# Optimization experiments

Hardware: AMD Instinct MI355X
Metric: run time of the kernel (lower is better)

The kernel has to match this reference:

```python
import jax, jax.numpy as jnp
import numpy as np
from functools import partial

TWO_PI = 2.0 * np.pi
H = 0.5          # frequency-grid spacing h
CG_ITERS = 50    # fixed CG iteration count (jit-friendly; matches max_cg_iter)
N_TRAIN = 100000
N_TEST = 20000
M_GRID = 64


def setup_inputs() -> dict:
    key = jax.random.key(0)
    k1, k2, k3, k4 = jax.random.split(key, 4)
    x = jax.random.uniform(k1, (N_TRAIN, 2), dtype=jnp.float32)          # nonuniform pts in [0,1]^2
    y = jax.random.normal(k2, (N_TRAIN,), dtype=jnp.float32)
    x_new = jax.random.uniform(k3, (N_TEST, 2), dtype=jnp.float32)
    # positive quadrature weights (Fourier-feature weights)
    ws = 0.5 + 0.5 * jax.random.uniform(k4, (M_GRID * M_GRID,), dtype=jnp.float32)
    sigma2 = 0.1 * jnp.ones((1,), dtype=jnp.float32)                     # noise variance
    return {"x": x, "y": y, "x_new": x_new, "ws": ws, "sigma2": sigma2, "mtot": M_GRID}


def _phase(pts_1d, freqs):
    # exp(2*pi*i * x * xi) : (N, K) complex64
    return jnp.exp(1j * (TWO_PI * pts_1d[:, None] * freqs[None, :]).astype(jnp.float32))


def _cg(A, b, iters):
    """Complex Hermitian-PD CG with fixed iteration count via lax.scan."""
    x0 = jnp.zeros_like(b)
    r0 = b
    rz0 = jnp.vdot(r0, r0).real

    def step(carry, _):
        xk, r, p, rz = carry
        Ap = A(p)
        denom = jnp.vdot(p, Ap).real
        alpha = rz / (denom + 1e-30)
        xk = xk + alpha * p
        r = r - alpha * Ap
        rz_new = jnp.vdot(r, r).real
        beta = rz_new / (rz + 1e-30)
        p = r + beta * p
        return (xk, r, p, rz_new), None

    (xk, _, _, _), _ = jax.lax.scan(step, (x0, r0, r0, rz0), None, length=iters)
    return xk


def reference(x, y, x_new, ws, sigma2, mtot):
    M = mtot
    S = 2 * M - 1
    # tensor-product frequency grid: xi_k = (k - M//2) * h per dimension
    xis_1d = (jnp.arange(M, dtype=jnp.float32) - M // 2) * H

    # ---- type-2 NUFFT adjoint (F^H y) computed separably: grid is tensor product
    E1 = _phase(x[:, 0], xis_1d)            # (N, M)
    E2 = _phase(x[:, 1], xis_1d)            # (N, M)
    Fy = jnp.einsum('na,nb->ab', jnp.conj(E1) * y[:, None].astype(jnp.complex64), jnp.conj(E2))  # (M, M)

    ws_g = ws.reshape(M, M).astype(jnp.complex64)
    rhs = ws_g * Fy                          # rhs = D F^H y

    # ---- type-1 NUFFT convolution vector v[p] = sum_n exp(2*pi*i*h*<p, x_n>), p in [-(M-1), M-1]^2
    p_1d = (jnp.arange(S, dtype=jnp.float32) - (M - 1)) * H
    G1 = _phase(x[:, 0], p_1d)              # (N, 2M-1)
    G2 = _phase(x[:, 1], p_1d)              # (N, 2M-1)
    v = jnp.einsum('na,nb->ab', G1, G2)     # (2M-1, 2M-1)
    # circularize so that index q = p mod S; v starts at p=-(M-1)
    v_circ = jnp.roll(v, shift=(-(M - 1), -(M - 1)), axis=(0, 1))
    Vf = jnp.fft.fftn(v_circ)

    def toeplitz_mv(u):                      # (T u)[k] = sum_j v[k-j] u[j], u: (M, M)
        Uf = jnp.fft.fftn(u, s=(S, S))
        full = jnp.fft.ifftn(Uf * Vf)
        return full[:M, :M]

    s2 = sigma2[0].astype(jnp.complex64)

    def A_mean(beta_flat):                   # A = D T D + sigma^2 I, acting on flat (M*M,)
        beta = beta_flat.reshape(M, M)
        out = ws_g * toeplitz_mv(ws_g * beta) + s2 * beta
        return out.reshape(-1)

    beta = _cg(A_mean, rhs.reshape(-1), CG_ITERS).reshape(M, M)

    # ---- posterior mean at test points: mu_b = Re( sum_{jk} exp(2 pi i <x_new_b, xi_jk>) * (ws*beta)[jk] )
    alpha_g = ws_g * beta                    # (M, M)
    T1 = _phase(x_new[:, 0], xis_1d)         # (B, M)
    T2 = _phase(x_new[:, 1], xis_1d)         # (B, M)
    tmp = jnp.einsum('jk,bk->bj', alpha_g, T2)   # (B, M)
    mu = jnp.real(jnp.sum(T1 * tmp, axis=1)).astype(jnp.float32)  # (B,)
    return mu
```

## Files before the change

kernel.cpp:

```cpp
#include <hip/hip_runtime.h>
#include <math.h>


typedef float f2 __attribute__((ext_vector_type(2)));
#define PB 16
#define RS 137

__device__ inline f2 f2s(float s) { return (f2){s, s}; }
__device__ inline f2 cmulf(f2 a, f2 b) {
    return (f2){a.x * b.x - a.y * b.y, a.x * b.y + a.y * b.x};
}
__device__ inline f2 cmulcf(f2 a, f2 b) {
    return (f2){a.x * b.x + a.y * b.y, a.y * b.x - a.x * b.y};
}
__device__ inline int cpad(int c) { return (c >> 4) * 17 + (c & 15); }

__device__ inline f2 phasef(float xv, float m, float scale) {
    double ang = (double)xv * (double)m;
    double r = ang - 2.0 * rint(ang * 0.5);
    float sn, cs;
    sincospif((float)r, &sn, &cs);
    return (f2){cs * scale, sn * scale};
}

__global__ __launch_bounds__(256, 2) void k_outer(const float* __restrict__ x,
                                                  const float* __restrict__ y,
                                                  float* __restrict__ pv,
                                                  float* __restrict__ pf,
                                                  int N, int cv, int cf)
{
    __shared__ f2 hs[PB][256];
    __shared__ float xs0[PB], xs1[PB], ys[PB];

    int bx = blockIdx.x;
    int t  = threadIdx.x;
    int ty = t >> 4, tx = t & 15;

    if (bx < cv) {
        int CP = (N + cv - 1) / cv;
        int n0 = bx * CP, n1 = min(N, n0 + CP);

        f2 acc[4][8];
        #pragma unroll
        for (int i = 0; i < 4; ++i)
            #pragma unroll
            for (int j = 0; j < 8; ++j) acc[i][j] = (f2){0.f, 0.f};

        for (int s = n0; s < n1; s += PB) {
            int cnt = min(PB, n1 - s);
            __syncthreads();
            if (t < cnt) {
                xs0[t] = x[2 * (s + t)];
                xs1[t] = x[2 * (s + t) + 1];
            }
            __syncthreads();
            for (int p = 0; p < cnt; ++p) {
                if (t < 192) {
                    f2 g;
                    if (t < 64)
                        g = phasef(xs0[p], (float)t, 1.f);
                    else
                        g = (t == 191) ? (f2){0.f, 0.f}
                                       : phasef(xs1[p], (float)(t - 127), 1.f);
                    hs[p][t] = g;
                }
            }
            __syncthreads();
            for (int p = 0; p < cnt; ++p) {
                f2 h1[4], h2[8], h2s[8];
                #pragma unroll
                for (int i = 0; i < 4; ++i) h1[i] = hs[p][ty * 4 + i];
                #pragma unroll
                for (int j = 0; j < 8; ++j) {
                    f2 b = hs[p][64 + tx + 16 * j];
                    h2[j] = b;
                    h2s[j] = (f2){-b.y, b.x};
                }
                #pragma unroll
                for (int i = 0; i < 4; ++i)
                    #pragma unroll
                    for (int j = 0; j < 8; ++j) {
                        acc[i][j] = acc[i][j] + f2s(h1[i].x) * h2[j];
                        acc[i][j] = acc[i][j] + f2s(h1[i].y) * h2s[j];
                    }
            }
        }
        __syncthreads();
        f2* out = (f2*)pv + (size_t)bx * 8192;
        #pragma unroll
        for (int i = 0; i < 4; ++i) {
            int a = ty * 4 + i;
            #pragma unroll
            for (int j = 0; j < 8; ++j)
                out[a * 128 + tx + 16 * j] = acc[i][j];
        }
    } else {
        int chunk = bx - cv;
        int CP = (N + cf - 1) / cf;
        int n0 = chunk * CP, n1 = min(N, n0 + CP);

        f2 acc[4][4];
        #pragma unroll
        for (int i = 0; i < 4; ++i)
            #pragma unroll
            for (int j = 0; j < 4; ++j) acc[i][j] = (f2){0.f, 0.f};

        for (int s = n0; s < n1; s += PB) {
            int cnt = min(PB, n1 - s);
            __syncthreads();
            if (t < cnt) {
                xs0[t] = x[2 * (s + t)];
                xs1[t] = x[2 * (s + t) + 1];
                ys[t]  = y[s + t];
            }
            __syncthreads();
            for (int p2 = 0; p2 < cnt; p2 += 2) {
                int p = p2 + (t >> 7);
                int c = t & 127;
                if (p < cnt) {
                    f2 g;
                    if (c < 64) g = phasef(xs0[p], (float)(32 - c), ys[p]);
                    else        g = phasef(xs1[p], (float)(32 - (c - 64)), 1.f);
                    hs[p][c] = g;
                }
            }
            __syncthreads();
            for (int p = 0; p < cnt; ++p) {
                f2 h1[4], h2[4], h2s[4];
                #pragma unroll
                for (int i = 0; i < 4; ++i) h1[i] = hs[p][ty * 4 + i];
                #pragma unroll
                for (int j = 0; j < 4; ++j) {
                    f2 b = hs[p][64 + tx + 16 * j];
                    h2[j] = b;
                    h2s[j] = (f2){-b.y, b.x};
                }
                #pragma unroll
                for (int i = 0; i < 4; ++i)
                    #pragma unroll
                    for (int j = 0; j < 4; ++j) {
                        acc[i][j] = acc[i][j] + f2s(h1[i].x) * h2[j];
                        acc[i][j] = acc[i][j] + f2s(h1[i].y) * h2s[j];
                    }
            }
        }
        __syncthreads();
        f2* out = (f2*)pf + (size_t)chunk * 4096;
        #pragma unroll
        for (int i = 0; i < 4; ++i) {
            int a = ty * 4 + i;
            #pragma unroll
            for (int j = 0; j < 4; ++j)
                out[a * 64 + tx + 16 * j] = acc[i][j];
        }
    }
}

__global__ __launch_bounds__(256) void k_reduce(const float* __restrict__ pv,
                                                const float* __restrict__ pf,
                                                const float* __restrict__ wsv,
                                                float* __restrict__ vcf,
                                                double2* __restrict__ rvec,
                                                int cv, int cf)
{
    int id = blockIdx.x * 256 + threadIdx.x;
    if (id < 65536) {
        int e = id >> 3, sl = id & 7;
        int cn = cv >> 3;
        const float* src = pv + (size_t)e * 2 + (size_t)(sl * cn) * 16384;
        float sx = 0.f, sy = 0.f;
        for (int c = 0; c < cn; ++c) { sx += src[0]; sy += src[1]; src += 16384; }
        int p1 = e >> 7, b = e & 127;
        int q2 = (b + 65) & 127;
        atomicAdd(&vcf[(p1 * 128 + q2) * 2],     sx);
        atomicAdd(&vcf[(p1 * 128 + q2) * 2 + 1], sy);
        if (p1 > 0) {
            int q1m = 128 - p1, q2m = (63 - b) & 127;
            atomicAdd(&vcf[(q1m * 128 + q2m) * 2],     sx);
            atomicAdd(&vcf[(q1m * 128 + q2m) * 2 + 1], -sy);
        }
    } else {
        int e = id - 65536;
        const float* s2p = pf + (size_t)e * 2;
        double fx = 0.0, fy2 = 0.0;
        for (int c = 0; c < cf; ++c) { fx += (double)s2p[0]; fy2 += (double)s2p[1]; s2p += 8192; }
        double w = (double)wsv[e];
        rvec[e] = make_double2(w * fx, w * fy2);
    }
}

#define TC1 0.92387953251128676f
#define TS1 0.38268343236508977f
#define TSQ 0.70710678118654752f

__device__ inline void bflyA_fwd(f2* L, const f2* tw, int b) {
    #pragma unroll
    for (int s = 0; s < 4; ++s) {
        f2 u0 = L[s], v0 = L[s + 4];
        L[s] = u0 + v0;
        L[s + 4] = cmulf(u0 - v0, tw[b + 16 * s]);
    }
    const int ss[4] = {0, 1, 4, 5};
    #pragma unroll
    for (int q = 0; q < 4; ++q) {
        int s = ss[q];
        f2 u0 = L[s], v0 = L[s + 2];
        L[s] = u0 + v0;
        L[s + 2] = cmulf(u0 - v0, tw[2 * b + 32 * (s & 1)]);
    }
    #pragma unroll
    for (int s = 0; s < 8; s += 2) {
        f2 u0 = L[s], v0 = L[s + 1];
        L[s] = u0 + v0;
        L[s + 1] = cmulf(u0 - v0, tw[4 * b]);
    }
}
__device__ inline void bflyA_inv(f2* L, const f2* tw, int b) {
    #pragma unroll
    for (int s = 0; s < 8; s += 2) {
        f2 u0 = L[s];
        f2 vw = cmulcf(L[s + 1], tw[4 * b]);
        L[s] = u0 + vw; L[s + 1] = u0 - vw;
    }
    const int ss[4] = {0, 1, 4, 5};
    #pragma unroll
    for (int q = 0; q < 4; ++q) {
        int s = ss[q];
        f2 u0 = L[s];
        f2 vw = cmulcf(L[s + 2], tw[2 * b + 32 * (s & 1)]);
        L[s] = u0 + vw; L[s + 2] = u0 - vw;
    }
    #pragma unroll
    for (int s = 0; s < 4; ++s) {
        f2 u0 = L[s];
        f2 vw = cmulcf(L[s + 4], tw[b + 16 * s]);
        L[s] = u0 + vw; L[s + 4] = u0 - vw;
    }
}
__device__ inline void bfly16_fwd(f2* M) {
    const float c8x[8]  = {1.f, TC1, TSQ, TS1, 0.f, -TS1, -TSQ, -TC1};
    const float c8y[8]  = {0.f, -TS1, -TSQ, -TC1, -1.f, -TC1, -TSQ, -TS1};
    const float c16x[4] = {1.f, TSQ, 0.f, -TSQ};
    const float c16y[4] = {0.f, -TSQ, -1.f, -TSQ};
    #pragma unroll
    for (int s = 0; s < 8; ++s) {
        f2 u0 = M[s], v0 = M[s + 8];
        M[s] = u0 + v0;
        M[s + 8] = cmulf(u0 - v0, (f2){c8x[s], c8y[s]});
    }
    #pragma unroll
    for (int q = 0; q < 8; ++q) {
        int s = (q & 3) + 8 * (q >> 2);
        f2 u0 = M[s], v0 = M[s + 4];
        M[s] = u0 + v0;
        M[s + 4] = cmulf(u0 - v0, (f2){c16x[s & 3], c16y[s & 3]});
    }
    #pragma unroll
    for (int q = 0; q < 8; ++q) {
        int s = (q & 1) + 4 * (q >> 1);
        f2 u0 = M[s], v0 = M[s + 2];
        M[s] = u0 + v0;
        f2 d = u0 - v0;
        M[s + 2] = (s & 1) ? (f2){d.y, -d.x} : d;
    }
    #pragma unroll
    for (int s = 0; s < 16; s += 2) {
        f2 u0 = M[s], v0 = M[s + 1];
        M[s] = u0 + v0; M[s + 1] = u0 - v0;
    }
}
__device__ inline void bfly16_inv(f2* M) {
    const float c8x[8]  = {1.f, TC1, TSQ, TS1, 0.f, -TS1, -TSQ, -TC1};
    const float c8y[8]  = {0.f, -TS1, -TSQ, -TC1, -1.f, -TC1, -TSQ, -TS1};
    const float c16x[4] = {1.f, TSQ, 0.f, -TSQ};
    const float c16y[4] = {0.f, -TSQ, -1.f, -TSQ};
    #pragma unroll
    for (int s = 0; s < 16; s += 2) {
        f2 u0 = M[s], v0 = M[s + 1];
        M[s] = u0 + v0; M[s + 1] = u0 - v0;
    }
    #pragma unroll
    for (int q = 0; q < 8; ++q) {
        int s = (q & 1) + 4 * (q >> 1);
        f2 u0 = M[s];
        f2 v0 = M[s + 2];
        f2 vw = (s & 1) ? (f2){-v0.y, v0.x} : v0;
        M[s] = u0 + vw; M[s + 2] = u0 - vw;
    }
    #pragma unroll
    for (int q = 0; q < 8; ++q) {
        int s = (q & 3) + 8 * (q >> 2);
        f2 u0 = M[s];
        f2 vw = cmulcf(M[s + 4], (f2){c16x[s & 3], c16y[s & 3]});
        M[s] = u0 + vw; M[s + 4] = u0 - vw;
    }
    #pragma unroll
    for (int s = 0; s < 8; ++s) {
        f2 u0 = M[s];
        f2 vw = cmulcf(M[s + 8], (f2){c8x[s], c8y[s]});
        M[s] = u0 + vw; M[s + 8] = u0 - vw;
    }
}

__device__ inline void f_rowA(f2* Z, const f2* tw, int tid, int nrows, bool zup) {
    for (int u = tid; u < nrows * 16; u += 1024) {
        int r = u >> 4, b = u & 15;
        f2* row = Z + r * RS;
        f2 L[8];
        #pragma unroll
        for (int s = 0; s < 4; ++s) L[s] = row[17 * s + b];
        if (zup) {
            #pragma unroll
            for (int s = 4; s < 8; ++s) L[s] = (f2){0.f, 0.f};
        } else {
            #pragma unroll
            for (int s = 4; s < 8; ++s) L[s] = row[17 * s + b];
        }
        bflyA_fwd(L, tw, b);
        #pragma unroll
        for (int s = 0; s < 8; ++s) row[17 * s + b] = L[s];
    }
}
__device__ inline void f_rowB(f2* Z, int tid, int nrows) {
    for (int u = tid; u < nrows * 8; u += 1024) {
        int r = u >> 3, g = u & 7;
        f2* blk = Z + r * RS + g * 17;
        f2 M[16];
        #pragma unroll
        for (int s = 0; s < 16; ++s) M[s] = blk[s];
        bfly16_fwd(M);
        #pragma unroll
        for (int s = 0; s < 16; ++s) blk[s] = M[s];
    }
}
__device__ inline void i_rowB(f2* Z, int tid, int nrows) {
    for (int u = tid; u < nrows * 8; u += 1024) {
        int r = u >> 3, g = u & 7;
        f2* blk = Z + r * RS + g * 17;
        f2 M[16];
        #pragma unroll
        for (int s = 0; s < 16; ++s) M[s] = blk[s];
        bfly16_inv(M);
        #pragma unroll
        for (int s = 0; s < 16; ++s) blk[s] = M[s];
    }
}
__device__ inline void f_colA(f2* Z, const f2* tw, int tid, bool zup) {
    for (int u = tid; u < 2048; u += 1024) {
        int c = u >> 4, b = u & 15;
        int cp = cpad(c);
        f2 L[8];
        #pragma unroll
        for (int s = 0; s < 4; ++s) L[s] = Z[(b + 16 * s) * RS + cp];
        if (zup) {
            #pragma unroll
            for (int s = 4; s < 8; ++s) L[s] = (f2){0.f, 0.f};
        } else {
            #pragma unroll
            for (int s = 4; s < 8; ++s) L[s] = Z[(b + 16 * s) * RS + cp];
        }
        bflyA_fwd(L, tw, b);
        #pragma unroll
        for (int s = 0; s < 8; ++s) Z[(b + 16 * s) * RS + cp] = L[s];
    }
}
__device__ inline void i_colA(f2* Z, const f2* tw, int tid) {
    for (int u = tid; u < 2048; u += 1024) {
        int c = u >> 4, b = u & 15;
        int cp = cpad(c);
        f2 L[8];
        #pragma unroll
        for (int s = 0; s < 8; ++s) L[s] = Z[(b + 16 * s) * RS + cp];
        bflyA_inv(L, tw, b);
        #pragma unroll
        for (int s = 0; s < 4; ++s) Z[(b + 16 * s) * RS + cp] = L[s];
    }
}
__device__ inline void f_colB(f2* Z, int tid) {
    int c = tid & 127, g = tid >> 7;
    f2* col = Z + g * 16 * RS + cpad(c);
    f2 M[16];
    #pragma unroll
    for (int s = 0; s < 16; ++s) M[s] = col[s * RS];
    bfly16_fwd(M);
    #pragma unroll
    for (int s = 0; s < 16; ++s) col[s * RS] = M[s];
}
__device__ inline void it_colB(f2* Z, const float* Vfg, int tid) {
    int c = tid & 127, g = tid >> 7;
    f2* col = Z + g * 16 * RS + cpad(c);
    const float* vf = Vfg + g * 16 * 128 + c;
    f2 M[16];
    #pragma unroll
    for (int s = 0; s < 16; ++s) M[s] = col[s * RS];
    bfly16_fwd(M);
    #pragma unroll
    for (int s = 0; s < 16; ++s) M[s] = M[s] * f2s(vf[s * 128]);
    bfly16_inv(M);
    #pragma unroll
    for (int s = 0; s < 16; ++s) col[s * RS] = M[s];
}

__device__ inline double blk_reduce(double v, double* red, int wid, int m) {
    #pragma unroll
    for (int off = 32; off > 0; off >>= 1) v += __shfl_down(v, off);
    if (m == 0) red[wid] = v;
    __syncthreads();
    double s = 0.0;
    #pragma unroll
    for (int i = 0; i < 16; ++i) s += red[i];
    return s;
}

__global__ __launch_bounds__(1024, 4) void k_cg_solve(
        const float* __restrict__ vcf, float* __restrict__ Vf,
        const double2* __restrict__ rvec, const float* __restrict__ wsv,
        const float* __restrict__ sig2, float* __restrict__ alg)
{
    __shared__ f2 Z[128 * RS];
    __shared__ f2 tw[64];
    __shared__ double redA[16], redB[16], redC[16];

    int tid = threadIdx.x;
    int wid = tid >> 6, m = tid & 63;
    int rr_ = tid >> 4, bb_ = tid & 15;

    if (tid < 64) {
        float sn, cs;
        sincospif(-(float)tid / 64.f, &sn, &cs);
        tw[tid] = (f2){cs, sn};
    }
    __syncthreads();

    for (int i = tid; i < 16384; i += 1024)
        Z[(i >> 7) * RS + cpad(i & 127)] = ((const f2*)vcf)[i];
    __syncthreads();
    f_rowA(Z, tw, tid, 128, false); __syncthreads();
    f_rowB(Z, tid, 128);            __syncthreads();
    f_colA(Z, tw, tid, false);      __syncthreads();
    f_colB(Z, tid);                 __syncthreads();
    for (int i = tid; i < 16384; i += 1024)
        Vf[i] = Z[(i >> 7) * RS + cpad(i & 127)].x * (1.f / 16384.f);
    __syncthreads();

    double2 pR[4], rR[4], xR[4];
    float wsr[4];
    double rzp = 0.0;
    #pragma unroll
    for (int s = 0; s < 4; ++s) {
        int e = rr_ * 64 + bb_ + (s << 4);
        double2 bv = rvec[e];
        pR[s] = bv; rR[s] = bv;
        xR[s] = make_double2(0.0, 0.0);
        wsr[s] = wsv[e];
        rzp += bv.x * bv.x + bv.y * bv.y;
    }
    double rz = blk_reduce(rzp, redC, wid, m);
    double s2 = (double)sig2[0];
    __syncthreads();

    for (int it = 0; it < 50; ++it) {
        {
            f2* row = Z + rr_ * RS;
            f2 L[8];
            #pragma unroll
            for (int s = 0; s < 4; ++s)
                L[s] = (f2){(float)((double)wsr[s] * pR[s].x),
                            (float)((double)wsr[s] * pR[s].y)};
            #pragma unroll
            for (int s = 4; s < 8; ++s) L[s] = (f2){0.f, 0.f};
            bflyA_fwd(L, tw, bb_);
            #pragma unroll
            for (int s = 0; s < 8; ++s) row[17 * s + bb_] = L[s];
        }
        __syncthreads();

        f_rowB(Z, tid, 64);                      __syncthreads();
        f_colA(Z, tw, tid, true);                __syncthreads();
        it_colB(Z, Vf, tid);                     __syncthreads();
        i_colA(Z, tw, tid);                      __syncthreads();
        i_rowB(Z, tid, 64);                      __syncthreads();

        f2 az[4];
        {
            f2* row = Z + rr_ * RS;
            f2 L[8];
            #pragma unroll
            for (int s = 0; s < 8; ++s) L[s] = row[17 * s + bb_];
            bflyA_inv(L, tw, bb_);
            #pragma unroll
            for (int s = 0; s < 4; ++s) az[s] = L[s];
        }
        double papp = 0.0;
        #pragma unroll
        for (int s = 0; s < 4; ++s) {
            double apx = (double)wsr[s] * (double)az[s].x + s2 * pR[s].x;
            double apy = (double)wsr[s] * (double)az[s].y + s2 * pR[s].y;
            papp += pR[s].x * apx + pR[s].y * apy;
        }
        double pap = blk_reduce(papp, redA, wid, m);
        double alpha = rz / (pap + 1e-30);

        double rrp = 0.0;
        #pragma unroll
        for (int s = 0; s < 4; ++s) {
            double apx = (double)wsr[s] * (double)az[s].x + s2 * pR[s].x;
            double apy = (double)wsr[s] * (double)az[s].y + s2 * pR[s].y;
            xR[s].x += alpha * pR[s].x; xR[s].y += alpha * pR[s].y;
            rR[s].x -= alpha * apx; rR[s].y -= alpha * apy;
            rrp += rR[s].x * rR[s].x + rR[s].y * rR[s].y;
        }
        double rzn = blk_reduce(rrp, redB, wid, m);
        double beta = rzn / (rz + 1e-30);
        rz = rzn;
        #pragma unroll
        for (int s = 0; s < 4; ++s) {
            pR[s].x = rR[s].x + beta * pR[s].x;
            pR[s].y = rR[s].y + beta * pR[s].y;
        }
    }

    #pragma unroll
    for (int s = 0; s < 4; ++s) {
        int e = rr_ * 64 + bb_ + (s << 4);
        ((f2*)alg)[e] = (f2){(float)((double)wsr[s] * xR[s].x),
                             (float)((double)wsr[s] * xR[s].y)};
    }
}

__global__ __launch_bounds__(64) void k_eval(const float* __restrict__ xnew,
                                             const float* __restrict__ alg,
                                             float* __restrict__ out, int B)
{
    __shared__ float2 al[4096];
    int t = threadIdx.x;
    int b = blockIdx.x * 64 + t;
    for (int i = t; i < 4096; i += 64) {
        f2 v = ((const f2*)alg)[i];
        al[i] = make_float2(v.x, v.y);
    }
    float x0 = 0.f, x1 = 0.f;
    if (b < B) { x0 = xnew[2 * b]; x1 = xnew[2 * b + 1]; }
    __syncthreads();
    double2 wstep; { double sn, cs; sincospi((double)x1, &sn, &cs); wstep = make_double2(cs, sn); }
    double2 e2_0;  { double sn, cs; sincospi(-32.0 * (double)x1, &sn, &cs); e2_0 = make_double2(cs, sn); }
    double2 w1;    { double sn, cs; sincospi((double)x0, &sn, &cs); w1 = make_double2(cs, sn); }
    double2 e1;    { double sn, cs; sincospi(-32.0 * (double)x0, &sn, &cs); e1 = make_double2(cs, sn); }
    double mu = 0.0;
    for (int jg = 0; jg < 4; ++jg) {
        float2 tacc[16];
        for (int q = 0; q < 16; ++q) tacc[q] = make_float2(0.f, 0.f);
        double2 e2 = e2_0;
        for (int k = 0; k < 64; ++k) {
            float2 e2f = make_float2((float)e2.x, (float)e2.y);
            for (int q = 0; q < 16; ++q) {
                int j = jg * 16 + q;
                float2 a = al[j * 64 + k];
                tacc[q].x += a.x * e2f.x - a.y * e2f.y;
                tacc[q].y += a.x * e2f.y + a.y * e2f.x;
            }
            e2 = make_double2(e2.x * wstep.x - e2.y * wstep.y,
                              e2.x * wstep.y + e2.y * wstep.x);
        }
        for (int q = 0; q < 16; ++q) {
            mu += e1.x * (double)tacc[q].x - e1.y * (double)tacc[q].y;
            e1 = make_double2(e1.x * w1.x - e1.y * w1.y,
                              e1.x * w1.y + e1.y * w1.x);
        }
    }
    if (b < B) out[b] = (float)mu;
}


extern "C" void kernel_launch(void* const* d_in, const int* in_sizes, int n_in,
                              void* d_out, int out_size, void* d_ws, size_t ws_size,
                              hipStream_t stream)
{
    const float* x    = (const float*)d_in[0];
    const float* y    = (const float*)d_in[1];
    const float* xnew = (const float*)d_in[2];
    const float* wsv  = (const float*)d_in[3];
    const float* sig2 = (const float*)d_in[4];
    int N = in_sizes[1];
    int B = in_sizes[2] / 2;

    char* base = (char*)d_ws;
    size_t o = 0;
    float*   vcf  = (float*)(base + o);   o += 131072;
    float*   Vf   = (float*)(base + o);   o += 65536;
    double2* rvec = (double2*)(base + o); o += 65536;
    float*   alg  = (float*)(base + o);   o += 32768;
    size_t avail = (ws_size > o) ? ws_size - o : 0;
    int cv = (int)(avail / 73728);
    if (cv > 768) cv = 768;
    if (cv < 16) cv = 16;
    cv &= ~15;
    int cf = cv / 4;
    float* pv = (float*)(base + o); o += (size_t)cv * 65536;
    float* pf = (float*)(base + o);

    hipMemsetAsync(vcf, 0, 131072, stream);

    k_outer<<<cv + cf, 256, 0, stream>>>(x, y, pv, pf, N, cv, cf);
    k_reduce<<<320, 256, 0, stream>>>(pv, pf, wsv, vcf, rvec, cv, cf);
    k_cg_solve<<<1, 1024, 0, stream>>>(vcf, Vf, rvec, wsv, sig2, alg);
    k_eval<<<(B + 63) / 64, 64, 0, stream>>>(xnew, alg, (float*)d_out, B);
}
```

Baseline: 1.143 ms.

## Run CG vector updates in fp32 and permute phase-table layout for contiguous reads

The CG solver's per-thread state (p, r, x) and its dot-product partials move from double to float, and the warp shuffle reductions run in float before a final double sum across waves. This is meant to cut fp64 ALU work and register pressure in the 50-iteration loop. Separately, the second-dimension phase table in the gridding kernel is stored in a permuted order so each thread reads its 8 entries contiguously. The fp32 CG may lose accuracy relative to the reference.

```diff
diff --git a/kernel.cpp b/kernel.cpp
--- a/kernel.cpp
+++ b/kernel.cpp
@@ -56,13 +56,14 @@
             __syncthreads();
             for (int p = 0; p < cnt; ++p) {
                 if (t < 192) {
-                    f2 g;
-                    if (t < 64)
-                        g = phasef(xs0[p], (float)t, 1.f);
-                    else
-                        g = (t == 191) ? (f2){0.f, 0.f}
-                                       : phasef(xs1[p], (float)(t - 127), 1.f);
-                    hs[p][t] = g;
+                    if (t < 64) {
+                        hs[p][t] = phasef(xs0[p], (float)t, 1.f);
+                    } else {
+                        int cc = t - 64;
+                        f2 g = (cc == 127) ? (f2){0.f, 0.f}
+                                           : phasef(xs1[p], (float)(cc - 63), 1.f);
+                        hs[p][64 + 8 * (cc & 15) + (cc >> 4)] = g;
+                    }
                 }
             }
             __syncthreads();
@@ -72,7 +73,7 @@
                 for (int i = 0; i < 4; ++i) h1[i] = hs[p][ty * 4 + i];
                 #pragma unroll
                 for (int j = 0; j < 8; ++j) {
-                    f2 b = hs[p][64 + tx + 16 * j];
+                    f2 b = hs[p][64 + 8 * tx + j];
                     h2[j] = b;
                     h2s[j] = (f2){-b.y, b.x};
                 }
@@ -411,6 +412,16 @@
     for (int i = 0; i < 16; ++i) s += red[i];
     return s;
 }
+__device__ inline double blk_reduce_f(float v, double* red, int wid, int m) {
+    #pragma unroll
+    for (int off = 32; off > 0; off >>= 1) v += __shfl_down(v, off);
+    if (m == 0) red[wid] = (double)v;
+    __syncthreads();
+    double s = 0.0;
+    #pragma unroll
+    for (int i = 0; i < 16; ++i) s += red[i];
+    return s;
+}
 
 __global__ __launch_bounds__(1024, 4) void k_cg_solve(
         const float* __restrict__ vcf, float* __restrict__ Vf,
@@ -443,20 +454,21 @@
         Vf[i] = Z[(i >> 7) * RS + cpad(i & 127)].x * (1.f / 16384.f);
     __syncthreads();
 
-    double2 pR[4], rR[4], xR[4];
+    f2 pR[4], rR[4], xR[4];
     float wsr[4];
-    double rzp = 0.0;
+    float rzp = 0.f;
     #pragma unroll
     for (int s = 0; s < 4; ++s) {
         int e = rr_ * 64 + bb_ + (s << 4);
         double2 bv = rvec[e];
-        pR[s] = bv; rR[s] = bv;
-        xR[s] = make_double2(0.0, 0.0);
+        f2 bf = (f2){(float)bv.x, (float)bv.y};
+        pR[s] = bf; rR[s] = bf;
+        xR[s] = (f2){0.f, 0.f};
         wsr[s] = wsv[e];
-        rzp += bv.x * bv.x + bv.y * bv.y;
-    }
-    double rz = blk_reduce(rzp, redC, wid, m);
-    double s2 = (double)sig2[0];
+        rzp += bf.x * bf.x + bf.y * bf.y;
+    }
+    double rz = blk_reduce_f(rzp, redC, wid, m);
+    float s2f = sig2[0];
     __syncthreads();
 
     for (int it = 0; it < 50; ++it) {
@@ -464,9 +476,7 @@
             f2* row = Z + rr_ * RS;
             f2 L[8];
             #pragma unroll
-            for (int s = 0; s < 4; ++s)
-                L[s] = (f2){(float)((double)wsr[s] * pR[s].x),
-                            (float)((double)wsr[s] * pR[s].y)};
+            for (int s = 0; s < 4; ++s) L[s] = f2s(wsr[s]) * pR[s];
             #pragma unroll
             for (int s = 4; s < 8; ++s) L[s] = (f2){0.f, 0.f};
             bflyA_fwd(L, tw, bb_);
@@ -481,7 +491,8 @@
         i_colA(Z, tw, tid);                      __syncthreads();
         i_rowB(Z, tid, 64);                      __syncthreads();
 
-        f2 az[4];
+        f2 ap[4];
+        float papp = 0.f;
         {
             f2* row = Z + rr_ * RS;
             f2 L[8];
@@ -489,42 +500,34 @@
             for (int s = 0; s < 8; ++s) L[s] = row[17 * s + bb_];
             bflyA_inv(L, tw, bb_);
             #pragma unroll
-            for (int s = 0; s < 4; ++s) az[s] = L[s];
-        }
-        double papp = 0.0;
+            for (int s = 0; s < 4; ++s) {
+                ap[s].x = wsr[s] * L[s].x + s2f * pR[s].x;
+                ap[s].y = wsr[s] * L[s].y + s2f * pR[s].y;
+                papp += pR[s].x * ap[s].x + pR[s].y * ap[s].y;
+            }
+        }
+        double pap = blk_reduce_f(papp, redA, wid, m);
+        float alpha = (float)(rz / (pap + 1e-30));
+
+        float rrp = 0.f;
         #pragma unroll
         for (int s = 0; s < 4; ++s) {
-            double apx = (double)wsr[s] * (double)az[s].x + s2 * pR[s].x;
-            double apy = (double)wsr[s] * (double)az[s].y + s2 * pR[s].y;
-            papp += pR[s].x * apx + pR[s].y * apy;
-        }
-        double pap = blk_reduce(papp, redA, wid, m);
-        double alpha = rz / (pap + 1e-30);
-
-        double rrp = 0.0;
-        #pragma unroll
-        for (int s = 0; s < 4; ++s) {
-            double apx = (double)wsr[s] * (double)az[s].x + s2 * pR[s].x;
-            double apy = (double)wsr[s] * (double)az[s].y + s2 * pR[s].y;
-            xR[s].x += alpha * pR[s].x; xR[s].y += alpha * pR[s].y;
-            rR[s].x -= alpha * apx; rR[s].y -= alpha * apy;
+            xR[s] = xR[s] + f2s(alpha) * pR[s];
+            rR[s] = rR[s] - f2s(alpha) * ap[s];
             rrp += rR[s].x * rR[s].x + rR[s].y * rR[s].y;
         }
-        double rzn = blk_reduce(rrp, redB, wid, m);
-        double beta = rzn / (rz + 1e-30);
+        double rzn = blk_reduce_f(rrp, redB, wid, m);
+        float beta = (float)(rzn / (rz + 1e-30));
         rz = rzn;
         #pragma unroll
-        for (int s = 0; s < 4; ++s) {
-            pR[s].x = rR[s].x + beta * pR[s].x;
-            pR[s].y = rR[s].y + beta * pR[s].y;
-        }
+        for (int s = 0; s < 4; ++s)
+            pR[s] = rR[s] + f2s(beta) * pR[s];
     }
 
     #pragma unroll
     for (int s = 0; s < 4; ++s) {
         int e = rr_ * 64 + bb_ + (s << 4);
-        ((f2*)alg)[e] = (f2){(float)((double)wsr[s] * xR[s].x),
-                             (float)((double)wsr[s] * xR[s].y)};
+        ((f2*)alg)[e] = f2s(wsr[s]) * xR[s];
     }
 }
 
```

Measured after the change: 944.9 us. 1.21x faster.
